# Kernel optimization log

Hardware: AMD Instinct MI355X
Metric: run time of the kernel (lower is better)

## Reference

```python
import jax, jax.numpy as jnp
import numpy as np

NEG_INF = -9e15  # matches the source's -9000000000000000.0 mask fill
ALPHA = 0.2      # leaky_relu negative slope


def setup_inputs() -> dict:
    key = jax.random.key(0)
    k1, k2, k3, k4 = jax.random.split(key, 4)
    B, N, C_IN, C_OUT, H = 2, 2048, 128, 128, 16
    c = C_OUT // H  # 8 per-head features; equals H//2 so source's a-slice is consistent
    node_feats = jax.random.normal(k1, (B, N, C_IN), dtype=jnp.float32)
    # random 0/1 adjacency with self-loops
    adj = jax.random.randint(k2, (B, N, N), 0, 2).astype(jnp.float32)
    adj = jnp.maximum(adj, jnp.eye(N, dtype=jnp.float32)[None])
    # glorot-uniform-ish params
    W = jax.random.normal(k3, (C_IN, H * c), dtype=jnp.float32) * np.sqrt(2.0 / (C_IN + H * c))
    b = jnp.zeros((H * c,), dtype=jnp.float32)
    a = jax.random.normal(k4, (H, 2 * c), dtype=jnp.float32) * np.sqrt(2.0 / (H + 2 * c))
    return {"node_feats": node_feats, "adj_matrix": adj, "W": W, "b": b, "a": a}


def reference(node_feats, adj_matrix, W, b, a):
    B, N = node_feats.shape[:2]
    H = a.shape[0]
    c = a.shape[1] // 2
    # projection + split into heads: [B, N, H, c]
    h = (node_feats @ W + b).reshape(B, N, H, c)
    # additive attention halves (source slices a along last axis)
    logit_parent = jnp.einsum('bnhc,hc->bnh', h, a[:, :c])
    logit_child = jnp.einsum('bnhc,hc->bnh', h, a[:, c:])
    # dense broadcast-add logits: [B, N(i), N(j), H]
    attn_logits = logit_parent[:, :, None, :] + logit_child[:, None, :, :]
    attn_logits = jax.nn.leaky_relu(attn_logits, negative_slope=ALPHA)
    attn_logits = jnp.where(adj_matrix[..., None] == 1.0, attn_logits, NEG_INF)
    attn_probs = jax.nn.softmax(attn_logits, axis=2)  # over source nodes j
    out = jnp.einsum('bijh,bjhc->bihc', attn_probs, h)
    out = out.reshape(B, N, H * c)  # concat_heads=True
    return out, adj_matrix
```

## Files before the change

### kernel.cpp

```cpp
#include <hip/hip_runtime.h>
#include <hip/hip_bf16.h>


#define B_   2
#define N_   2048
#define CIN_ 128
#define H_   16

typedef _Float16 h2  __attribute__((ext_vector_type(2)));
typedef _Float16 v8h __attribute__((ext_vector_type(8)));
typedef float    v4f __attribute__((ext_vector_type(4)));

#define SC6 0.015625f

__device__ inline h2 pk_f16(float a, float b) {
  return __builtin_bit_cast(h2, __builtin_amdgcn_cvt_pkrtz(a, b));
}
__device__ inline unsigned as_u32(h2 v) { return __builtin_bit_cast(unsigned, v); }
__device__ inline h2 as_h2(unsigned u) { return __builtin_bit_cast(h2, u); }

__global__ __launch_bounds__(128) void proj_kernel(
    const float* __restrict__ nf, const float* __restrict__ W,
    const float* __restrict__ bias, const float* __restrict__ a,
    unsigned* __restrict__ hQ, unsigned* __restrict__ qI,
    float* __restrict__ lpT, unsigned* __restrict__ ones) {
  const int row0 = blockIdx.x * 4;
  const int t    = threadIdx.x;
  if (blockIdx.x == 0) {
    ones[t] = 0x3C003C00u; ones[t + 128] = 0x3C003C00u;
    ones[t + 256] = 0x3C003C00u; ones[t + 384] = 0x3C003C00u;
  }
  __shared__ float sNf[4][CIN_];
  ((float4*)&sNf[0][0])[t] = ((const float4*)(nf + (long)row0 * CIN_))[t];
  __syncthreads();
  float acc[4];
  const float bv = bias[t];
#pragma unroll
  for (int r = 0; r < 4; ++r) acc[r] = bv;
#pragma unroll 8
  for (int k = 0; k < CIN_; ++k) {
    const float w = W[k * 128 + t];
#pragma unroll
    for (int r = 0; r < 4; ++r) acc[r] = fmaf(sNf[r][k], w, acc[r]);
  }
  const int h = t >> 3, kc = t & 7;
  const int b = row0 >> 11, n0 = row0 & (N_ - 1);
  const int bh = b * H_ + h;
  const int cdw = n0 >> 1;
  uint2 hv;
  hv.x = as_u32(pk_f16(acc[0], acc[1]));
  hv.y = as_u32(pk_f16(acc[2], acc[3]));
  *(uint2*)(hQ + ((long)(bh * 8 + kc)) * (N_ / 2) + cdw) = hv;

  const float ap = a[h * 16 + kc], ac = a[h * 16 + 8 + kc];
  float lpv[4], lcv[4];
#pragma unroll
  for (int r = 0; r < 4; ++r) {
    float x = acc[r] * ap, y = acc[r] * ac;
#pragma unroll
    for (int s = 1; s < 8; s <<= 1) {
      x += __shfl_xor(x, s);
      y += __shfl_xor(y, s);
    }
    lpv[r] = x; lcv[r] = y;
  }
  if (kc == 0) {
    float4 l0 = {lpv[0], lpv[1], lpv[2], lpv[3]};
    *(float4*)(lpT + (long)bh * N_ + n0) = l0;
    uint2 q1, q2;
    q1.x = as_u32(pk_f16(__expf(lcv[0]) * SC6, __expf(lcv[1]) * SC6));
    q1.y = as_u32(pk_f16(__expf(lcv[2]) * SC6, __expf(lcv[3]) * SC6));
    q2.x = as_u32(pk_f16(__expf(0.2f * lcv[0]) * SC6, __expf(0.2f * lcv[1]) * SC6));
    q2.y = as_u32(pk_f16(__expf(0.2f * lcv[2]) * SC6, __expf(0.2f * lcv[3]) * SC6));
    const int addr = bh * 2048 + (cdw >> 4) * 32 + ((cdw >> 2) & 3) * 8;
    const int off  = cdw & 3;
    *(uint2*)(qI + addr + off)     = q1;
    *(uint2*)(qI + addr + 4 + off) = q2;
  }
}

__global__ __launch_bounds__(512) void attn_kernel(
    const float* __restrict__ adj, const unsigned* __restrict__ hQ,
    const unsigned* __restrict__ qI, const float* __restrict__ lpT,
    const unsigned* __restrict__ ones, float* __restrict__ pA,
    float* __restrict__ pL, float* __restrict__ adj_out) {
  const int jq   = blockIdx.x & 3;
  const int rest = blockIdx.x >> 2;
  const int b    = rest >> 6;
  const int i0   = (rest & 63) * 32;
  const int tid  = threadIdx.x;
  const int w    = tid >> 6;
  const int lane = tid & 63;

  __shared__ uint4    sA[2048];
  __shared__ unsigned sQ[8192];

  {
    const int head = tid >> 5;
    const int off  = (tid & 31) * 16;
    const uint4* src = (const uint4*)(qI + (b * H_ + head) * 2048 + jq * 512 + off);
    uint4* dst = (uint4*)(sQ + head * 512 + off);
    dst[0] = src[0]; dst[1] = src[1]; dst[2] = src[2]; dst[3] = src[3];
  }
  {
    const long aoff = (long)(b * N_ + i0) * N_ + jq * 512;
    const float* abase = adj + aoff;
    float* obase = adj_out + aoff;
    float4 fa[4], fb[4];
    int rowv[4], ccv[4];
#pragma unroll
    for (int s = 0; s < 4; ++s) {
      const int D = s * 512 + tid;
      const int u = D >> 10, loc = D & 1023;
      const int mm = loc & 15, qc = loc >> 4;
      ccv[s] = (qc >> 2) * 32 + (qc & 3) * 8;
      rowv[s] = u * 16 + mm;
      fa[s] = *(const float4*)(abase + (long)rowv[s] * N_ + ccv[s]);
      fb[s] = *(const float4*)(abase + (long)rowv[s] * N_ + ccv[s] + 4);
    }
#pragma unroll
    for (int s = 0; s < 4; ++s) {
      const int D = s * 512 + tid;
      uint4 uu;
      uu.x = as_u32(pk_f16(fa[s].x, fa[s].y)); uu.y = as_u32(pk_f16(fa[s].z, fa[s].w));
      uu.z = as_u32(pk_f16(fb[s].x, fb[s].y)); uu.w = as_u32(pk_f16(fb[s].z, fb[s].w));
      sA[D] = uu;
      *(float4*)(obase + (long)rowv[s] * N_ + ccv[s])     = fa[s];
      *(float4*)(obase + (long)rowv[s] * N_ + ccv[s] + 4) = fb[s];
    }
  }
  __syncthreads();

  const int m  = lane & 15;
  const int q  = lane >> 4;
  const int bh0 = b * H_ + w;
  const int bh1 = bh0 + 8;

  const float lpa0 = lpT[(long)bh0 * N_ + i0 + m];
  const float lpb0 = lpT[(long)bh0 * N_ + i0 + 16 + m];
  const float lpa1 = lpT[(long)bh1 * N_ + i0 + m];
  const float lpb1 = lpT[(long)bh1 * N_ + i0 + 16 + m];
  const h2 P1a0 = pk_f16(__expf(lpa0) * SC6, __expf(lpa0) * SC6);
  const h2 P2a0 = pk_f16(__expf(0.2f * lpa0) * SC6, __expf(0.2f * lpa0) * SC6);
  const h2 P1b0 = pk_f16(__expf(lpb0) * SC6, __expf(lpb0) * SC6);
  const h2 P2b0 = pk_f16(__expf(0.2f * lpb0) * SC6, __expf(0.2f * lpb0) * SC6);
  const h2 P1a1 = pk_f16(__expf(lpa1) * SC6, __expf(lpa1) * SC6);
  const h2 P2a1 = pk_f16(__expf(0.2f * lpa1) * SC6, __expf(0.2f * lpa1) * SC6);
  const h2 P1b1 = pk_f16(__expf(lpb1) * SC6, __expf(lpb1) * SC6);
  const h2 P2b1 = pk_f16(__expf(0.2f * lpb1) * SC6, __expf(0.2f * lpb1) * SC6);

  const unsigned* sq0 = sQ + w * 512 + q * 8;
  const unsigned* sq1 = sQ + (w + 8) * 512 + q * 8;
  const unsigned* hp0 = (m < 8)
      ? hQ + ((long)(bh0 * 8 + m)) * (N_ / 2) + jq * 256 + q * 4
      : ones + q * 4;
  const unsigned* hp1 = (m < 8)
      ? hQ + ((long)(bh1 * 8 + m)) * (N_ / 2) + jq * 256 + q * 4
      : ones + q * 4;

  v4f acc0a = {0.f, 0.f, 0.f, 0.f}, acc1a = {0.f, 0.f, 0.f, 0.f};
  v4f acc0b = {0.f, 0.f, 0.f, 0.f}, acc1b = {0.f, 0.f, 0.f, 0.f};

  uint4 h0[4], h1[4];
#pragma unroll
  for (int d = 0; d < 4; ++d) {
    h0[d] = *(const uint4*)(hp0 + d * 16);
    h1[d] = *(const uint4*)(hp1 + d * 16);
  }

  for (int t4 = 0; t4 < 4; ++t4) {
#pragma unroll
    for (int s = 0; s < 4; ++s) {
      const int ch = t4 * 4 + s;
      const int pf = ((ch + 4) & 15) * 16;
      const uint4 n0 = *(const uint4*)(hp0 + pf);
      const uint4 n1 = *(const uint4*)(hp1 + pf);

      const uint4 q1c0 = *(const uint4*)(sq0 + ch * 32);
      const uint4 q2c0 = *(const uint4*)(sq0 + ch * 32 + 4);
      const uint4 q1c1 = *(const uint4*)(sq1 + ch * 32);
      const uint4 q2c1 = *(const uint4*)(sq1 + ch * 32 + 4);
      const uint4 Av0 = sA[ch * 64 + lane];
      const uint4 Av1 = sA[1024 + ch * 64 + lane];

      {
        const h2 Q1x = as_h2(q1c0.x), Q1y = as_h2(q1c0.y), Q1z = as_h2(q1c0.z), Q1w = as_h2(q1c0.w);
        const h2 Q2x = as_h2(q2c0.x), Q2y = as_h2(q2c0.y), Q2z = as_h2(q2c0.z), Q2w = as_h2(q2c0.w);
        const v8h bf = __builtin_bit_cast(v8h, h0[s]);
        const uint4 af0 = {
          as_u32(__builtin_elementwise_max(P1a0 * Q1x, P2a0 * Q2x) * as_h2(Av0.x)),
          as_u32(__builtin_elementwise_max(P1a0 * Q1y, P2a0 * Q2y) * as_h2(Av0.y)),
          as_u32(__builtin_elementwise_max(P1a0 * Q1z, P2a0 * Q2z) * as_h2(Av0.z)),
          as_u32(__builtin_elementwise_max(P1a0 * Q1w, P2a0 * Q2w) * as_h2(Av0.w))};
        acc0a = __builtin_amdgcn_mfma_f32_16x16x32_f16(
            __builtin_bit_cast(v8h, af0), bf, acc0a, 0, 0, 0);
        const uint4 af1 = {
          as_u32(__builtin_elementwise_max(P1b0 * Q1x, P2b0 * Q2x) * as_h2(Av1.x)),
          as_u32(__builtin_elementwise_max(P1b0 * Q1y, P2b0 * Q2y) * as_h2(Av1.y)),
          as_u32(__builtin_elementwise_max(P1b0 * Q1z, P2b0 * Q2z) * as_h2(Av1.z)),
          as_u32(__builtin_elementwise_max(P1b0 * Q1w, P2b0 * Q2w) * as_h2(Av1.w))};
        acc1a = __builtin_amdgcn_mfma_f32_16x16x32_f16(
            __builtin_bit_cast(v8h, af1), bf, acc1a, 0, 0, 0);
      }
      {
        const h2 Q1x = as_h2(q1c1.x), Q1y = as_h2(q1c1.y), Q1z = as_h2(q1c1.z), Q1w = as_h2(q1c1.w);
        const h2 Q2x = as_h2(q2c1.x), Q2y = as_h2(q2c1.y), Q2z = as_h2(q2c1.z), Q2w = as_h2(q2c1.w);
        const v8h bf = __builtin_bit_cast(v8h, h1[s]);
        const uint4 af0 = {
          as_u32(__builtin_elementwise_max(P1a1 * Q1x, P2a1 * Q2x) * as_h2(Av0.x)),
          as_u32(__builtin_elementwise_max(P1a1 * Q1y, P2a1 * Q2y) * as_h2(Av0.y)),
          as_u32(__builtin_elementwise_max(P1a1 * Q1z, P2a1 * Q2z) * as_h2(Av0.z)),
          as_u32(__builtin_elementwise_max(P1a1 * Q1w, P2a1 * Q2w) * as_h2(Av0.w))};
        acc0b = __builtin_amdgcn_mfma_f32_16x16x32_f16(
            __builtin_bit_cast(v8h, af0), bf, acc0b, 0, 0, 0);
        const uint4 af1 = {
          as_u32(__builtin_elementwise_max(P1b1 * Q1x, P2b1 * Q2x) * as_h2(Av1.x)),
          as_u32(__builtin_elementwise_max(P1b1 * Q1y, P2b1 * Q2y) * as_h2(Av1.y)),
          as_u32(__builtin_elementwise_max(P1b1 * Q1z, P2b1 * Q2z) * as_h2(Av1.z)),
          as_u32(__builtin_elementwise_max(P1b1 * Q1w, P2b1 * Q2w) * as_h2(Av1.w))};
        acc1b = __builtin_amdgcn_mfma_f32_16x16x32_f16(
            __builtin_bit_cast(v8h, af1), bf, acc1b, 0, 0, 0);
      }
      h0[s] = n0; h1[s] = n1;
    }
  }

#pragma unroll
  for (int g = 0; g < 2; ++g) {
    const int hw = g * 8 + w;
#pragma unroll
    for (int u = 0; u < 2; ++u) {
      const v4f av = g ? (u ? acc1b : acc0b) : (u ? acc1a : acc0a);
#pragma unroll
      for (int r = 0; r < 4; ++r) {
        const int gidx = (b * N_ + i0 + u * 16 + q * 4 + r) * H_ + hw;
        if (m < 8)  pA[jq * 524288 + (long)gidx * 8 + m] = av[r];
        if (m == 8) pL[jq * 65536 + gidx] = av[r];
      }
    }
  }
}

__global__ __launch_bounds__(512) void combine_kernel(
    const float* __restrict__ pA, const float* __restrict__ pL,
    float* __restrict__ out) {
  const int g = blockIdx.x * 512 + threadIdx.x;
  const int gl = g >> 3;
  const float s = pL[gl] + pL[gl + 65536] + pL[gl + 131072] + pL[gl + 196608];
  const float v = pA[g] + pA[g + 524288] + pA[g + 1048576] + pA[g + 1572864];
  out[g] = v / s;
}

extern "C" void kernel_launch(void* const* d_in, const int* in_sizes, int n_in,
                              void* d_out, int out_size, void* d_ws, size_t ws_size,
                              hipStream_t stream) {
  const float* nf   = (const float*)d_in[0];
  const float* adj  = (const float*)d_in[1];
  const float* W    = (const float*)d_in[2];
  const float* bias = (const float*)d_in[3];
  const float* a    = (const float*)d_in[4];

  float* out     = (float*)d_out;
  float* adj_out = out + (long)B_ * N_ * H_ * 8;

  unsigned* ws   = (unsigned*)d_ws;
  unsigned* hQ   = ws;
  unsigned* qI   = ws + 262144;
  float*    lpT  = (float*)(ws + 327680);
  unsigned* ones = ws + 393216;
  float*    pA   = (float*)(ws + 393728);
  float*    pL   = (float*)(ws + 2490880);

  hipLaunchKernelGGL(proj_kernel, dim3(B_ * N_ / 4), dim3(128), 0, stream,
                     nf, W, bias, a, hQ, qI, lpT, ones);
  hipLaunchKernelGGL(attn_kernel, dim3(B_ * (N_ / 32) * 4), dim3(512), 0,
                     stream, adj, hQ, qI, lpT, ones, pA, pL, adj_out);
  hipLaunchKernelGGL(combine_kernel, dim3(1024), dim3(512), 0, stream,
                     pA, pL, out);
}
```

Before: 125.0 us.

## Halve attention row tile and replace f16 adjacency multiply with byte bitmask AND

The attention kernel now processes 16 query rows per block instead of 32, doubling the grid. The adjacency tile in shared memory is stored as byte masks (0x00/0xFF per element, expanded by v_perm into 16-bit masks) rather than f16 values. The mask is applied with a bitwise AND instead of an f16 multiply, and launch bounds request 6 waves per SIMD. This cuts LDS footprint and VALU work per element and raises occupancy, but the mask conversion assumes adjacency values are exactly 0 or 1, and each block now reloads the h and q operands for half as many rows.

```diff
diff --git a/kernel.cpp b/kernel.cpp
--- a/kernel.cpp
+++ b/kernel.cpp
@@ -18,6 +18,12 @@
 }
 __device__ inline unsigned as_u32(h2 v) { return __builtin_bit_cast(unsigned, v); }
 __device__ inline h2 as_h2(unsigned u) { return __builtin_bit_cast(h2, u); }
+
+__device__ inline unsigned mask4(float4 f) {
+  unsigned r = (unsigned)f.x | ((unsigned)f.y << 8) |
+               ((unsigned)f.z << 16) | ((unsigned)f.w << 24);
+  return (r << 8) - r;
+}
 
 __global__ __launch_bounds__(128) void proj_kernel(
     const float* __restrict__ nf, const float* __restrict__ W,
@@ -79,20 +85,20 @@
   }
 }
 
-__global__ __launch_bounds__(512) void attn_kernel(
+__global__ __launch_bounds__(512, 6) void attn_kernel(
     const float* __restrict__ adj, const unsigned* __restrict__ hQ,
     const unsigned* __restrict__ qI, const float* __restrict__ lpT,
     const unsigned* __restrict__ ones, float* __restrict__ pA,
     float* __restrict__ pL, float* __restrict__ adj_out) {
   const int jq   = blockIdx.x & 3;
   const int rest = blockIdx.x >> 2;
-  const int b    = rest >> 6;
-  const int i0   = (rest & 63) * 32;
+  const int b    = rest >> 7;
+  const int i0   = (rest & 127) * 16;
   const int tid  = threadIdx.x;
   const int w    = tid >> 6;
   const int lane = tid & 63;
 
-  __shared__ uint4    sA[2048];
+  __shared__ uint2    sAm[1024];
   __shared__ unsigned sQ[8192];
 
   {
@@ -106,25 +112,22 @@
     const long aoff = (long)(b * N_ + i0) * N_ + jq * 512;
     const float* abase = adj + aoff;
     float* obase = adj_out + aoff;
-    float4 fa[4], fb[4];
-    int rowv[4], ccv[4];
-#pragma unroll
-    for (int s = 0; s < 4; ++s) {
+    float4 fa[2], fb[2];
+    int rowv[2], ccv[2];
+#pragma unroll
+    for (int s = 0; s < 2; ++s) {
       const int D = s * 512 + tid;
-      const int u = D >> 10, loc = D & 1023;
-      const int mm = loc & 15, qc = loc >> 4;
+      const int mm = D & 15, qc = D >> 4;
       ccv[s] = (qc >> 2) * 32 + (qc & 3) * 8;
-      rowv[s] = u * 16 + mm;
-      fa[s] = *(const float4*)(abase + (long)rowv[s] * N_ + ccv[s]);
-      fb[s] = *(const float4*)(abase + (long)rowv[s] * N_ + ccv[s] + 4);
-    }
-#pragma unroll
-    for (int s = 0; s < 4; ++s) {
+      rowv[s] = mm;
+      fa[s] = *(const float4*)(abase + (long)mm * N_ + ccv[s]);
+      fb[s] = *(const float4*)(abase + (long)mm * N_ + ccv[s] + 4);
+    }
+#pragma unroll
+    for (int s = 0; s < 2; ++s) {
       const int D = s * 512 + tid;
-      uint4 uu;
-      uu.x = as_u32(pk_f16(fa[s].x, fa[s].y)); uu.y = as_u32(pk_f16(fa[s].z, fa[s].w));
-      uu.z = as_u32(pk_f16(fb[s].x, fb[s].y)); uu.w = as_u32(pk_f16(fb[s].z, fb[s].w));
-      sA[D] = uu;
+      uint2 mv; mv.x = mask4(fa[s]); mv.y = mask4(fb[s]);
+      sAm[D] = mv;
       *(float4*)(obase + (long)rowv[s] * N_ + ccv[s])     = fa[s];
       *(float4*)(obase + (long)rowv[s] * N_ + ccv[s] + 4) = fb[s];
     }
@@ -136,18 +139,12 @@
   const int bh0 = b * H_ + w;
   const int bh1 = bh0 + 8;
 
-  const float lpa0 = lpT[(long)bh0 * N_ + i0 + m];
-  const float lpb0 = lpT[(long)bh0 * N_ + i0 + 16 + m];
-  const float lpa1 = lpT[(long)bh1 * N_ + i0 + m];
-  const float lpb1 = lpT[(long)bh1 * N_ + i0 + 16 + m];
-  const h2 P1a0 = pk_f16(__expf(lpa0) * SC6, __expf(lpa0) * SC6);
-  const h2 P2a0 = pk_f16(__expf(0.2f * lpa0) * SC6, __expf(0.2f * lpa0) * SC6);
-  const h2 P1b0 = pk_f16(__expf(lpb0) * SC6, __expf(lpb0) * SC6);
-  const h2 P2b0 = pk_f16(__expf(0.2f * lpb0) * SC6, __expf(0.2f * lpb0) * SC6);
-  const h2 P1a1 = pk_f16(__expf(lpa1) * SC6, __expf(lpa1) * SC6);
-  const h2 P2a1 = pk_f16(__expf(0.2f * lpa1) * SC6, __expf(0.2f * lpa1) * SC6);
-  const h2 P1b1 = pk_f16(__expf(lpb1) * SC6, __expf(lpb1) * SC6);
-  const h2 P2b1 = pk_f16(__expf(0.2f * lpb1) * SC6, __expf(0.2f * lpb1) * SC6);
+  const float lp0 = lpT[(long)bh0 * N_ + i0 + m];
+  const float lp1 = lpT[(long)bh1 * N_ + i0 + m];
+  const float e10 = __expf(lp0) * SC6, e20 = __expf(0.2f * lp0) * SC6;
+  const float e11 = __expf(lp1) * SC6, e21 = __expf(0.2f * lp1) * SC6;
+  const h2 P10 = pk_f16(e10, e10), P20 = pk_f16(e20, e20);
+  const h2 P11 = pk_f16(e11, e11), P21 = pk_f16(e21, e21);
 
   const unsigned* sq0 = sQ + w * 512 + q * 8;
   const unsigned* sq1 = sQ + (w + 8) * 512 + q * 8;
@@ -158,21 +155,18 @@
       ? hQ + ((long)(bh1 * 8 + m)) * (N_ / 2) + jq * 256 + q * 4
       : ones + q * 4;
 
-  v4f acc0a = {0.f, 0.f, 0.f, 0.f}, acc1a = {0.f, 0.f, 0.f, 0.f};
-  v4f acc0b = {0.f, 0.f, 0.f, 0.f}, acc1b = {0.f, 0.f, 0.f, 0.f};
-
-  uint4 h0[4], h1[4];
-#pragma unroll
-  for (int d = 0; d < 4; ++d) {
-    h0[d] = *(const uint4*)(hp0 + d * 16);
-    h1[d] = *(const uint4*)(hp1 + d * 16);
-  }
-
-  for (int t4 = 0; t4 < 4; ++t4) {
-#pragma unroll
-    for (int s = 0; s < 4; ++s) {
-      const int ch = t4 * 4 + s;
-      const int pf = ((ch + 4) & 15) * 16;
+  v4f acc0 = {0.f, 0.f, 0.f, 0.f};
+  v4f acc1 = {0.f, 0.f, 0.f, 0.f};
+
+  uint4 h0[2], h1[2];
+  h0[0] = *(const uint4*)(hp0);      h1[0] = *(const uint4*)(hp1);
+  h0[1] = *(const uint4*)(hp0 + 16); h1[1] = *(const uint4*)(hp1 + 16);
+
+  for (int t2 = 0; t2 < 8; ++t2) {
+#pragma unroll
+    for (int s = 0; s < 2; ++s) {
+      const int ch = t2 * 2 + s;
+      const int pf = ((ch + 2) & 15) * 16;
       const uint4 n0 = *(const uint4*)(hp0 + pf);
       const uint4 n1 = *(const uint4*)(hp1 + pf);
 
@@ -180,46 +174,32 @@
       const uint4 q2c0 = *(const uint4*)(sq0 + ch * 32 + 4);
       const uint4 q1c1 = *(const uint4*)(sq1 + ch * 32);
       const uint4 q2c1 = *(const uint4*)(sq1 + ch * 32 + 4);
-      const uint4 Av0 = sA[ch * 64 + lane];
-      const uint4 Av1 = sA[1024 + ch * 64 + lane];
+
+      const uint2 Mv = sAm[ch * 64 + lane];
+      const unsigned ma = __builtin_amdgcn_perm(Mv.x, Mv.x, 0x01010000u);
+      const unsigned mb = __builtin_amdgcn_perm(Mv.x, Mv.x, 0x03030202u);
+      const unsigned mc = __builtin_amdgcn_perm(Mv.y, Mv.y, 0x01010000u);
+      const unsigned md = __builtin_amdgcn_perm(Mv.y, Mv.y, 0x03030202u);
 
       {
-        const h2 Q1x = as_h2(q1c0.x), Q1y = as_h2(q1c0.y), Q1z = as_h2(q1c0.z), Q1w = as_h2(q1c0.w);
-        const h2 Q2x = as_h2(q2c0.x), Q2y = as_h2(q2c0.y), Q2z = as_h2(q2c0.z), Q2w = as_h2(q2c0.w);
         const v8h bf = __builtin_bit_cast(v8h, h0[s]);
-        const uint4 af0 = {
-          as_u32(__builtin_elementwise_max(P1a0 * Q1x, P2a0 * Q2x) * as_h2(Av0.x)),
-          as_u32(__builtin_elementwise_max(P1a0 * Q1y, P2a0 * Q2y) * as_h2(Av0.y)),
-          as_u32(__builtin_elementwise_max(P1a0 * Q1z, P2a0 * Q2z) * as_h2(Av0.z)),
-          as_u32(__builtin_elementwise_max(P1a0 * Q1w, P2a0 * Q2w) * as_h2(Av0.w))};
-        acc0a = __builtin_amdgcn_mfma_f32_16x16x32_f16(
-            __builtin_bit_cast(v8h, af0), bf, acc0a, 0, 0, 0);
-        const uint4 af1 = {
-          as_u32(__builtin_elementwise_max(P1b0 * Q1x, P2b0 * Q2x) * as_h2(Av1.x)),
-          as_u32(__builtin_elementwise_max(P1b0 * Q1y, P2b0 * Q2y) * as_h2(Av1.y)),
-          as_u32(__builtin_elementwise_max(P1b0 * Q1z, P2b0 * Q2z) * as_h2(Av1.z)),
-          as_u32(__builtin_elementwise_max(P1b0 * Q1w, P2b0 * Q2w) * as_h2(Av1.w))};
-        acc1a = __builtin_amdgcn_mfma_f32_16x16x32_f16(
-            __builtin_bit_cast(v8h, af1), bf, acc1a, 0, 0, 0);
+        const uint4 af = {
+          as_u32(__builtin_elementwise_max(P10 * as_h2(q1c0.x), P20 * as_h2(q2c0.x))) & ma,
+          as_u32(__builtin_elementwise_max(P10 * as_h2(q1c0.y), P20 * as_h2(q2c0.y))) & mb,
+          as_u32(__builtin_elementwise_max(P10 * as_h2(q1c0.z), P20 * as_h2(q2c0.z))) & mc,
+          as_u32(__builtin_elementwise_max(P10 * as_h2(q1c0.w), P20 * as_h2(q2c0.w))) & md};
+        acc0 = __builtin_amdgcn_mfma_f32_16x16x32_f16(
+            __builtin_bit_cast(v8h, af), bf, acc0, 0, 0, 0);
       }
       {
-        const h2 Q1x = as_h2(q1c1.x), Q1y = as_h2(q1c1.y), Q1z = as_h2(q1c1.z), Q1w = as_h2(q1c1.w);
-        const h2 Q2x = as_h2(q2c1.x), Q2y = as_h2(q2c1.y), Q2z = as_h2(q2c1.z), Q2w = as_h2(q2c1.w);
         const v8h bf = __builtin_bit_cast(v8h, h1[s]);
-        const uint4 af0 = {
-          as_u32(__builtin_elementwise_max(P1a1 * Q1x, P2a1 * Q2x) * as_h2(Av0.x)),
-          as_u32(__builtin_elementwise_max(P1a1 * Q1y, P2a1 * Q2y) * as_h2(Av0.y)),
-          as_u32(__builtin_elementwise_max(P1a1 * Q1z, P2a1 * Q2z) * as_h2(Av0.z)),
-          as_u32(__builtin_elementwise_max(P1a1 * Q1w, P2a1 * Q2w) * as_h2(Av0.w))};
-        acc0b = __builtin_amdgcn_mfma_f32_16x16x32_f16(
-            __builtin_bit_cast(v8h, af0), bf, acc0b, 0, 0, 0);
-        const uint4 af1 = {
-          as_u32(__builtin_elementwise_max(P1b1 * Q1x, P2b1 * Q2x) * as_h2(Av1.x)),
-          as_u32(__builtin_elementwise_max(P1b1 * Q1y, P2b1 * Q2y) * as_h2(Av1.y)),
-          as_u32(__builtin_elementwise_max(P1b1 * Q1z, P2b1 * Q2z) * as_h2(Av1.z)),
-          as_u32(__builtin_elementwise_max(P1b1 * Q1w, P2b1 * Q2w) * as_h2(Av1.w))};
-        acc1b = __builtin_amdgcn_mfma_f32_16x16x32_f16(
-            __builtin_bit_cast(v8h, af1), bf, acc1b, 0, 0, 0);
+        const uint4 af = {
+          as_u32(__builtin_elementwise_max(P11 * as_h2(q1c1.x), P21 * as_h2(q2c1.x))) & ma,
+          as_u32(__builtin_elementwise_max(P11 * as_h2(q1c1.y), P21 * as_h2(q2c1.y))) & mb,
+          as_u32(__builtin_elementwise_max(P11 * as_h2(q1c1.z), P21 * as_h2(q2c1.z))) & mc,
+          as_u32(__builtin_elementwise_max(P11 * as_h2(q1c1.w), P21 * as_h2(q2c1.w))) & md};
+        acc1 = __builtin_amdgcn_mfma_f32_16x16x32_f16(
+            __builtin_bit_cast(v8h, af), bf, acc1, 0, 0, 0);
       }
       h0[s] = n0; h1[s] = n1;
     }
@@ -228,15 +208,12 @@
 #pragma unroll
   for (int g = 0; g < 2; ++g) {
     const int hw = g * 8 + w;
-#pragma unroll
-    for (int u = 0; u < 2; ++u) {
-      const v4f av = g ? (u ? acc1b : acc0b) : (u ? acc1a : acc0a);
-#pragma unroll
-      for (int r = 0; r < 4; ++r) {
-        const int gidx = (b * N_ + i0 + u * 16 + q * 4 + r) * H_ + hw;
-        if (m < 8)  pA[jq * 524288 + (long)gidx * 8 + m] = av[r];
-        if (m == 8) pL[jq * 65536 + gidx] = av[r];
-      }
+    const v4f av = g ? acc1 : acc0;
+#pragma unroll
+    for (int r = 0; r < 4; ++r) {
+      const int gidx = (b * N_ + i0 + q * 4 + r) * H_ + hw;
+      if (m < 8)  pA[jq * 524288 + (long)gidx * 8 + m] = av[r];
+      if (m == 8) pL[jq * 65536 + gidx] = av[r];
     }
   }
 }
@@ -273,7 +250,7 @@
 
   hipLaunchKernelGGL(proj_kernel, dim3(B_ * N_ / 4), dim3(128), 0, stream,
                      nf, W, bias, a, hQ, qI, lpT, ones);
-  hipLaunchKernelGGL(attn_kernel, dim3(B_ * (N_ / 32) * 4), dim3(512), 0,
+  hipLaunchKernelGGL(attn_kernel, dim3(B_ * (N_ / 16) * 4), dim3(512), 0,
                      stream, adj, hQ, qI, lpT, ones, pA, pL, adj_out);
   hipLaunchKernelGGL(combine_kernel, dim3(1024), dim3(512), 0, stream,
                      pA, pL, out);
```

After: 127.0 us. No clear change (+1.5%).

## Stream adjacency tiles directly from global into registers instead of staging in LDS

Applied to the files above, without the earlier changes.

Drops the shared-memory staging buffer for the adjacency tile. Each wave now loads the fp32 adjacency rows it needs straight from global memory into registers, double-buffered one chunk ahead, and converts them to fp16 on the fly. Wave 0 alone writes the adj_out copy. This removes the up-front load/convert/store phase, the barrier that followed it, and 32KB of LDS. The cost is that all eight waves now read the same adjacency rows from global/L2, roughly eight times the adjacency read traffic through cache, and the prefetch depth for h shrinks from four chunks to two.

```diff
diff --git a/kernel.cpp b/kernel.cpp
--- a/kernel.cpp
+++ b/kernel.cpp
@@ -92,7 +92,6 @@
   const int w    = tid >> 6;
   const int lane = tid & 63;
 
-  __shared__ uint4    sA[2048];
   __shared__ unsigned sQ[8192];
 
   {
@@ -102,34 +101,6 @@
     uint4* dst = (uint4*)(sQ + head * 512 + off);
     dst[0] = src[0]; dst[1] = src[1]; dst[2] = src[2]; dst[3] = src[3];
   }
-  {
-    const long aoff = (long)(b * N_ + i0) * N_ + jq * 512;
-    const float* abase = adj + aoff;
-    float* obase = adj_out + aoff;
-    float4 fa[4], fb[4];
-    int rowv[4], ccv[4];
-#pragma unroll
-    for (int s = 0; s < 4; ++s) {
-      const int D = s * 512 + tid;
-      const int u = D >> 10, loc = D & 1023;
-      const int mm = loc & 15, qc = loc >> 4;
-      ccv[s] = (qc >> 2) * 32 + (qc & 3) * 8;
-      rowv[s] = u * 16 + mm;
-      fa[s] = *(const float4*)(abase + (long)rowv[s] * N_ + ccv[s]);
-      fb[s] = *(const float4*)(abase + (long)rowv[s] * N_ + ccv[s] + 4);
-    }
-#pragma unroll
-    for (int s = 0; s < 4; ++s) {
-      const int D = s * 512 + tid;
-      uint4 uu;
-      uu.x = as_u32(pk_f16(fa[s].x, fa[s].y)); uu.y = as_u32(pk_f16(fa[s].z, fa[s].w));
-      uu.z = as_u32(pk_f16(fb[s].x, fb[s].y)); uu.w = as_u32(pk_f16(fb[s].z, fb[s].w));
-      sA[D] = uu;
-      *(float4*)(obase + (long)rowv[s] * N_ + ccv[s])     = fa[s];
-      *(float4*)(obase + (long)rowv[s] * N_ + ccv[s] + 4) = fb[s];
-    }
-  }
-  __syncthreads();
 
   const int m  = lane & 15;
   const int q  = lane >> 4;
@@ -149,6 +120,13 @@
   const h2 P1b1 = pk_f16(__expf(lpb1) * SC6, __expf(lpb1) * SC6);
   const h2 P2b1 = pk_f16(__expf(0.2f * lpb1) * SC6, __expf(0.2f * lpb1) * SC6);
 
+  const long rbase0 = (long)(b * N_ + i0 + m) * N_ + jq * 512 + q * 8;
+  const long rbase1 = rbase0 + 16L * N_;
+  const float* aR0 = adj + rbase0;
+  const float* aR1 = adj + rbase1;
+  float* oR0 = adj_out + rbase0;
+  float* oR1 = adj_out + rbase1;
+
   const unsigned* sq0 = sQ + w * 512 + q * 8;
   const unsigned* sq1 = sQ + (w + 8) * 512 + q * 8;
   const unsigned* hp0 = (m < 8)
@@ -161,68 +139,87 @@
   v4f acc0a = {0.f, 0.f, 0.f, 0.f}, acc1a = {0.f, 0.f, 0.f, 0.f};
   v4f acc0b = {0.f, 0.f, 0.f, 0.f}, acc1b = {0.f, 0.f, 0.f, 0.f};
 
-  uint4 h0[4], h1[4];
-#pragma unroll
-  for (int d = 0; d < 4; ++d) {
-    h0[d] = *(const uint4*)(hp0 + d * 16);
-    h1[d] = *(const uint4*)(hp1 + d * 16);
-  }
-
-  for (int t4 = 0; t4 < 4; ++t4) {
-#pragma unroll
-    for (int s = 0; s < 4; ++s) {
-      const int ch = t4 * 4 + s;
-      const int pf = ((ch + 4) & 15) * 16;
-      const uint4 n0 = *(const uint4*)(hp0 + pf);
-      const uint4 n1 = *(const uint4*)(hp1 + pf);
-
-      const uint4 q1c0 = *(const uint4*)(sq0 + ch * 32);
-      const uint4 q2c0 = *(const uint4*)(sq0 + ch * 32 + 4);
-      const uint4 q1c1 = *(const uint4*)(sq1 + ch * 32);
-      const uint4 q2c1 = *(const uint4*)(sq1 + ch * 32 + 4);
-      const uint4 Av0 = sA[ch * 64 + lane];
-      const uint4 Av1 = sA[1024 + ch * 64 + lane];
-
-      {
-        const h2 Q1x = as_h2(q1c0.x), Q1y = as_h2(q1c0.y), Q1z = as_h2(q1c0.z), Q1w = as_h2(q1c0.w);
-        const h2 Q2x = as_h2(q2c0.x), Q2y = as_h2(q2c0.y), Q2z = as_h2(q2c0.z), Q2w = as_h2(q2c0.w);
-        const v8h bf = __builtin_bit_cast(v8h, h0[s]);
-        const uint4 af0 = {
-          as_u32(__builtin_elementwise_max(P1a0 * Q1x, P2a0 * Q2x) * as_h2(Av0.x)),
-          as_u32(__builtin_elementwise_max(P1a0 * Q1y, P2a0 * Q2y) * as_h2(Av0.y)),
-          as_u32(__builtin_elementwise_max(P1a0 * Q1z, P2a0 * Q2z) * as_h2(Av0.z)),
-          as_u32(__builtin_elementwise_max(P1a0 * Q1w, P2a0 * Q2w) * as_h2(Av0.w))};
-        acc0a = __builtin_amdgcn_mfma_f32_16x16x32_f16(
-            __builtin_bit_cast(v8h, af0), bf, acc0a, 0, 0, 0);
-        const uint4 af1 = {
-          as_u32(__builtin_elementwise_max(P1b0 * Q1x, P2b0 * Q2x) * as_h2(Av1.x)),
-          as_u32(__builtin_elementwise_max(P1b0 * Q1y, P2b0 * Q2y) * as_h2(Av1.y)),
-          as_u32(__builtin_elementwise_max(P1b0 * Q1z, P2b0 * Q2z) * as_h2(Av1.z)),
-          as_u32(__builtin_elementwise_max(P1b0 * Q1w, P2b0 * Q2w) * as_h2(Av1.w))};
-        acc1a = __builtin_amdgcn_mfma_f32_16x16x32_f16(
-            __builtin_bit_cast(v8h, af1), bf, acc1a, 0, 0, 0);
-      }
-      {
-        const h2 Q1x = as_h2(q1c1.x), Q1y = as_h2(q1c1.y), Q1z = as_h2(q1c1.z), Q1w = as_h2(q1c1.w);
-        const h2 Q2x = as_h2(q2c1.x), Q2y = as_h2(q2c1.y), Q2z = as_h2(q2c1.z), Q2w = as_h2(q2c1.w);
-        const v8h bf = __builtin_bit_cast(v8h, h1[s]);
-        const uint4 af0 = {
-          as_u32(__builtin_elementwise_max(P1a1 * Q1x, P2a1 * Q2x) * as_h2(Av0.x)),
-          as_u32(__builtin_elementwise_max(P1a1 * Q1y, P2a1 * Q2y) * as_h2(Av0.y)),
-          as_u32(__builtin_elementwise_max(P1a1 * Q1z, P2a1 * Q2z) * as_h2(Av0.z)),
-          as_u32(__builtin_elementwise_max(P1a1 * Q1w, P2a1 * Q2w) * as_h2(Av0.w))};
-        acc0b = __builtin_amdgcn_mfma_f32_16x16x32_f16(
-            __builtin_bit_cast(v8h, af0), bf, acc0b, 0, 0, 0);
-        const uint4 af1 = {
-          as_u32(__builtin_elementwise_max(P1b1 * Q1x, P2b1 * Q2x) * as_h2(Av1.x)),
-          as_u32(__builtin_elementwise_max(P1b1 * Q1y, P2b1 * Q2y) * as_h2(Av1.y)),
-          as_u32(__builtin_elementwise_max(P1b1 * Q1z, P2b1 * Q2z) * as_h2(Av1.z)),
-          as_u32(__builtin_elementwise_max(P1b1 * Q1w, P2b1 * Q2w) * as_h2(Av1.w))};
-        acc1b = __builtin_amdgcn_mfma_f32_16x16x32_f16(
-            __builtin_bit_cast(v8h, af1), bf, acc1b, 0, 0, 0);
-      }
-      h0[s] = n0; h1[s] = n1;
-    }
+  float4 A0[2], Bb0[2], A1[2], Bb1[2];
+  A0[0]  = *(const float4*)(aR0);
+  Bb0[0] = *(const float4*)(aR0 + 4);
+  A1[0]  = *(const float4*)(aR1);
+  Bb1[0] = *(const float4*)(aR1 + 4);
+  uint4 h0[2], h1[2];
+  h0[0] = *(const uint4*)(hp0);      h1[0] = *(const uint4*)(hp1);
+  h0[1] = *(const uint4*)(hp0 + 16); h1[1] = *(const uint4*)(hp1 + 16);
+
+  __syncthreads();
+
+#pragma unroll
+  for (int ch = 0; ch < 16; ++ch) {
+    const int p  = ch & 1;
+    const int nn = (ch + 1) & 1;
+    const int nco = ((ch + 1) & 15) * 32;
+    A0[nn]  = *(const float4*)(aR0 + nco);
+    Bb0[nn] = *(const float4*)(aR0 + nco + 4);
+    A1[nn]  = *(const float4*)(aR1 + nco);
+    Bb1[nn] = *(const float4*)(aR1 + nco + 4);
+    const int pf = ((ch + 2) & 15) * 16;
+    const uint4 nh0 = *(const uint4*)(hp0 + pf);
+    const uint4 nh1 = *(const uint4*)(hp1 + pf);
+
+    if (w == 0) {
+      *(float4*)(oR0 + ch * 32)     = A0[p];
+      *(float4*)(oR0 + ch * 32 + 4) = Bb0[p];
+      *(float4*)(oR1 + ch * 32)     = A1[p];
+      *(float4*)(oR1 + ch * 32 + 4) = Bb1[p];
+    }
+
+    uint4 Av0, Av1;
+    Av0.x = as_u32(pk_f16(A0[p].x,  A0[p].y));  Av0.y = as_u32(pk_f16(A0[p].z,  A0[p].w));
+    Av0.z = as_u32(pk_f16(Bb0[p].x, Bb0[p].y)); Av0.w = as_u32(pk_f16(Bb0[p].z, Bb0[p].w));
+    Av1.x = as_u32(pk_f16(A1[p].x,  A1[p].y));  Av1.y = as_u32(pk_f16(A1[p].z,  A1[p].w));
+    Av1.z = as_u32(pk_f16(Bb1[p].x, Bb1[p].y)); Av1.w = as_u32(pk_f16(Bb1[p].z, Bb1[p].w));
+
+    const uint4 q1c0 = *(const uint4*)(sq0 + ch * 32);
+    const uint4 q2c0 = *(const uint4*)(sq0 + ch * 32 + 4);
+    const uint4 q1c1 = *(const uint4*)(sq1 + ch * 32);
+    const uint4 q2c1 = *(const uint4*)(sq1 + ch * 32 + 4);
+
+    {
+      const h2 Q1x = as_h2(q1c0.x), Q1y = as_h2(q1c0.y), Q1z = as_h2(q1c0.z), Q1w = as_h2(q1c0.w);
+      const h2 Q2x = as_h2(q2c0.x), Q2y = as_h2(q2c0.y), Q2z = as_h2(q2c0.z), Q2w = as_h2(q2c0.w);
+      const v8h bf = __builtin_bit_cast(v8h, h0[p]);
+      const uint4 af0 = {
+        as_u32(__builtin_elementwise_max(P1a0 * Q1x, P2a0 * Q2x) * as_h2(Av0.x)),
+        as_u32(__builtin_elementwise_max(P1a0 * Q1y, P2a0 * Q2y) * as_h2(Av0.y)),
+        as_u32(__builtin_elementwise_max(P1a0 * Q1z, P2a0 * Q2z) * as_h2(Av0.z)),
+        as_u32(__builtin_elementwise_max(P1a0 * Q1w, P2a0 * Q2w) * as_h2(Av0.w))};
+      acc0a = __builtin_amdgcn_mfma_f32_16x16x32_f16(
+          __builtin_bit_cast(v8h, af0), bf, acc0a, 0, 0, 0);
+      const uint4 af1 = {
+        as_u32(__builtin_elementwise_max(P1b0 * Q1x, P2b0 * Q2x) * as_h2(Av1.x)),
+        as_u32(__builtin_elementwise_max(P1b0 * Q1y, P2b0 * Q2y) * as_h2(Av1.y)),
+        as_u32(__builtin_elementwise_max(P1b0 * Q1z, P2b0 * Q2z) * as_h2(Av1.z)),
+        as_u32(__builtin_elementwise_max(P1b0 * Q1w, P2b0 * Q2w) * as_h2(Av1.w))};
+      acc1a = __builtin_amdgcn_mfma_f32_16x16x32_f16(
+          __builtin_bit_cast(v8h, af1), bf, acc1a, 0, 0, 0);
+    }
+    {
+      const h2 Q1x = as_h2(q1c1.x), Q1y = as_h2(q1c1.y), Q1z = as_h2(q1c1.z), Q1w = as_h2(q1c1.w);
+      const h2 Q2x = as_h2(q2c1.x), Q2y = as_h2(q2c1.y), Q2z = as_h2(q2c1.z), Q2w = as_h2(q2c1.w);
+      const v8h bf = __builtin_bit_cast(v8h, h1[p]);
+      const uint4 af0 = {
+        as_u32(__builtin_elementwise_max(P1a1 * Q1x, P2a1 * Q2x) * as_h2(Av0.x)),
+        as_u32(__builtin_elementwise_max(P1a1 * Q1y, P2a1 * Q2y) * as_h2(Av0.y)),
+        as_u32(__builtin_elementwise_max(P1a1 * Q1z, P2a1 * Q2z) * as_h2(Av0.z)),
+        as_u32(__builtin_elementwise_max(P1a1 * Q1w, P2a1 * Q2w) * as_h2(Av0.w))};
+      acc0b = __builtin_amdgcn_mfma_f32_16x16x32_f16(
+          __builtin_bit_cast(v8h, af0), bf, acc0b, 0, 0, 0);
+      const uint4 af1 = {
+        as_u32(__builtin_elementwise_max(P1b1 * Q1x, P2b1 * Q2x) * as_h2(Av1.x)),
+        as_u32(__builtin_elementwise_max(P1b1 * Q1y, P2b1 * Q2y) * as_h2(Av1.y)),
+        as_u32(__builtin_elementwise_max(P1b1 * Q1z, P2b1 * Q2z) * as_h2(Av1.z)),
+        as_u32(__builtin_elementwise_max(P1b1 * Q1w, P2b1 * Q2w) * as_h2(Av1.w))};
+      acc1b = __builtin_amdgcn_mfma_f32_16x16x32_f16(
+          __builtin_bit_cast(v8h, af1), bf, acc1b, 0, 0, 0);
+    }
+    h0[p] = nh0; h1[p] = nh1;
   }
 
 #pragma unroll
```

After: 141.3 us. 13.0% more time.
